# Performance work log

Measured on AMD Instinct MI355X. Metric: run time of the kernel, lower is better.

## Reference

```python
import jax, jax.numpy as jnp
import numpy as np

B, N, C, H, L = 4, 1024, 1152, 16, 120
D = C // H
HID = 4 * C
EPS = 1e-6


def _ln(x):
    m = jnp.mean(x, axis=-1, keepdims=True)
    v = jnp.var(x, axis=-1, keepdims=True)
    return (x - m) * jax.lax.rsqrt(v + EPS)


def _attend(q, k, v):
    # q:(B,H,Nq,D) k,v:(B,H,Nk,D)
    scale = D ** -0.5
    s = jnp.einsum('bhnd,bhmd->bhnm', q, k) * scale
    p = jax.nn.softmax(s, axis=-1)
    o = jnp.einsum('bhnm,bhmd->bhnd', p, v)
    return o.transpose(0, 2, 1, 3).reshape(q.shape[0], q.shape[2], C)


def setup_inputs() -> dict:
    key = jax.random.key(0)
    ks = jax.random.split(key, 20)
    g = lambda i, shape, s=0.02: jax.random.normal(ks[i], shape, jnp.float32) * s
    return {
        'x': jax.random.normal(ks[0], (B, N, C), jnp.float32),
        'y': jax.random.normal(ks[1], (B, L, C), jnp.float32),
        't': jax.random.normal(ks[2], (B, 6 * C), jnp.float32),
        'sst': jax.random.normal(ks[3], (6, C), jnp.float32) / C ** 0.5,
        'qkv_w': g(4, (C, 3 * C)), 'qkv_b': jnp.zeros((3 * C,), jnp.float32),
        'proj_w': g(5, (C, C)), 'proj_b': jnp.zeros((C,), jnp.float32),
        'q_w': g(6, (C, C)), 'q_b': jnp.zeros((C,), jnp.float32),
        'kv_w': g(7, (C, 2 * C)), 'kv_b': jnp.zeros((2 * C,), jnp.float32),
        'cproj_w': g(8, (C, C)), 'cproj_b': jnp.zeros((C,), jnp.float32),
        'fc1_w': g(9, (C, HID)), 'fc1_b': jnp.zeros((HID,), jnp.float32),
        'fc2_w': g(10, (HID, C)), 'fc2_b': jnp.zeros((C,), jnp.float32),
    }


def reference(x, y, t, sst, qkv_w, qkv_b, proj_w, proj_b, q_w, q_b,
              kv_w, kv_b, cproj_w, cproj_b, fc1_w, fc1_b, fc2_w, fc2_b):
    mods = sst[None] + t.reshape(B, 6, C)  # (B,6,C)
    sh_msa, sc_msa, g_msa, sh_mlp, sc_mlp, g_mlp = [mods[:, i:i + 1] for i in range(6)]

    # --- self attention with adaLN modulation ---
    h = _ln(x) * (1 + sc_msa) + sh_msa
    qkv = (h @ qkv_w + qkv_b).reshape(B, N, 3, H, D).transpose(2, 0, 3, 1, 4)
    attn_out = _attend(qkv[0], qkv[1], qkv[2]) @ proj_w + proj_b
    x = x + g_msa * attn_out

    # --- cross attention (batched cond, no mask) ---
    q = (x @ q_w + q_b).reshape(B, N, H, D).transpose(0, 2, 1, 3)
    kv = (y @ kv_w + kv_b).reshape(B, L, 2, H, D).transpose(2, 0, 3, 1, 4)
    x = x + (_attend(q, kv[0], kv[1]) @ cproj_w + cproj_b)

    # --- MLP with adaLN modulation ---
    h = _ln(x) * (1 + sc_mlp) + sh_mlp
    h = jax.nn.gelu(h @ fc1_w + fc1_b, approximate=True) @ fc2_w + fc2_b
    x = x + g_mlp * h
    return x
```

## Files before the change

### kernel.cpp

```cpp
#include <hip/hip_runtime.h>
#include <hip/hip_bf16.h>
#include <stdint.h>

typedef __hip_bfloat16 BT;
typedef __bf16 bf16x8 __attribute__((ext_vector_type(8)));
typedef float f32x4 __attribute__((ext_vector_type(4)));

constexpr int kB = 4, kN = 1024, kC = 1152, kH = 16, kL = 120, kD = 72, kDp = 96;
constexpr int kHid = 4608, kBN = 4096, kZ = 64;
constexpr float kScale = 0.11785113019775793f;

__global__ void detect_dtype(const void* xin, int* flag) {
  __shared__ int cnt;
  if (threadIdx.x == 0) cnt = 0;
  __syncthreads();
  const BT* xb = (const BT*)xin;
  int local = 0;
  for (int i = threadIdx.x; i < 4096; i += 256) {
    float v = __bfloat162float(xb[i]);
    if (!(fabsf(v) <= 1e3f)) local++;
  }
  atomicAdd(&cnt, local);
  __syncthreads();
  if (threadIdx.x == 0) *flag = (cnt > 8) ? 1 : 0;
}

struct ConvSeg {
  const void* src;
  BT* dst;
  long long n;
};
struct ConvArgs {
  ConvSeg seg[10];
  int nseg;
};
__global__ void convert_all(ConvArgs a, const int* __restrict__ flag) {
  const int f = *flag;
  long long i = (long long)blockIdx.x * 256 + threadIdx.x;
#pragma unroll
  for (int s = 0; s < 10; ++s) {
    if (s >= a.nseg) return;
    if (i < a.seg[s].n) {
      a.seg[s].dst[i] = f ? __float2bfloat16(((const float*)a.seg[s].src)[i])
                          : ((const BT*)a.seg[s].src)[i];
      return;
    }
    i -= a.seg[s].n;
  }
}

__global__ void encode_ws(float* out, long long n, float c) {
  long long i = (long long)blockIdx.x * 256 + threadIdx.x;
  if (i < n) out[i] = c;
}

__device__ __forceinline__ void gl_lds16(const BT* g, BT* l) {
  __builtin_amdgcn_global_load_lds(
      (const __attribute__((address_space(1))) uint32_t*)g,
      (__attribute__((address_space(3))) uint32_t*)l, 16, 0, 0);
}

__device__ __forceinline__ bf16x8 ds_read128(const BT* p) {
  f32x4 r;
  auto lp = (const __attribute__((address_space(3))) f32x4*)p;
  asm volatile("ds_read_b128 %0, %1" : "=v"(r) : "v"(lp));
  return __builtin_bit_cast(bf16x8, r);
}

template <int EP>
__global__ __launch_bounds__(256, 2) void gemm_p3(
    const BT* __restrict__ A, const BT* __restrict__ Bm, const BT* __restrict__ bias,
    void* __restrict__ Cout, int M, int Nc, int K, int lda, int ldb, int ldc,
    long long sA, long long sB, long long sC) {
  __shared__ __align__(16) BT As[3][128 * 64];
  __shared__ __align__(16) BT Bs[3][64 * 64];
  A += (long long)blockIdx.z * sA;
  Bm += (long long)blockIdx.z * sB;

  const int gx = gridDim.x, nwg = gx * gridDim.y;
  int id = blockIdx.y * gx + blockIdx.x;
  {
    const int q = nwg >> 3, r = nwg & 7;
    const int xcd = id & 7, pos = id >> 3;
    const int base = (xcd < r) ? xcd * (q + 1) : r * (q + 1) + (xcd - r) * q;
    id = base + pos;
  }
  const int m0 = (id / gx) * 128, n0 = (id % gx) * 64;

  const int lane = threadIdx.x & 63, w = threadIdx.x >> 6;
  const int l15 = lane & 15;
  const int srow = lane >> 3;
  const int ssrc = ((lane & 7) ^ srow) * 8;
  const int wm = (w >> 1) * 64, wn = (w & 1) * 32;

  const BT* gsp[6];
  int eoff[6];
  bool isA[6];
#pragma unroll
  for (int i = 0; i < 6; ++i) {
    const int gidx = w * 6 + i;
    const int u = gidx >> 2, q = gidx & 3;
    if (u < 4) {
      int rr = m0 + u * 32 + q * 8 + srow;
      if (rr >= M) rr = M - 1;
      gsp[i] = A + (long long)rr * lda + ssrc;
      eoff[i] = u * 2048 + q * 512;
      isA[i] = true;
    } else {
      int rr = n0 + (u - 4) * 32 + q * 8 + srow;
      if (rr >= Nc) rr = Nc - 1;
      gsp[i] = Bm + (long long)rr * ldb + ssrc;
      eoff[i] = (u - 4) * 2048 + q * 512;
      isA[i] = false;
    }
  }

  auto stage = [&](int bb, int k0) {
#pragma unroll
    for (int i = 0; i < 6; ++i)
      gl_lds16(gsp[i] + k0, isA[i] ? &As[bb][eoff[i]] : &Bs[bb][eoff[i]]);
  };

  const int rsw = l15 & 7;
  const int ch0 = ((lane >> 4) ^ rsw) * 8;
  const int ch1 = ((4 | (lane >> 4)) ^ rsw) * 8;

  f32x4 acc[4][2] = {};

  const int nk = K >> 6;
  stage(0, 0);
  stage(1, 64);
  asm volatile("s_waitcnt vmcnt(6)" ::: "memory");
  __builtin_amdgcn_s_barrier();

  int cur = 0;
  for (int t = 0; t < nk; ++t) {
    const bool more = (t + 2 < nk);
    if (more) {
      int nb = cur + 2;
      if (nb >= 3) nb -= 3;
      stage(nb, (t + 2) << 6);
    }
    const BT* Ab = &As[cur][0];
    const BT* Bb = &Bs[cur][0];
    bf16x8 af[4][2], bf[2][2];
#pragma unroll
    for (int i = 0; i < 4; ++i) {
      const int row = wm + i * 16 + l15;
      af[i][0] = ds_read128(&Ab[row * 64 + ch0]);
      af[i][1] = ds_read128(&Ab[row * 64 + ch1]);
    }
#pragma unroll
    for (int j = 0; j < 2; ++j) {
      const int row = wn + j * 16 + l15;
      bf[j][0] = ds_read128(&Bb[row * 64 + ch0]);
      bf[j][1] = ds_read128(&Bb[row * 64 + ch1]);
    }
    asm volatile("s_waitcnt lgkmcnt(0)" ::: "memory");
    __builtin_amdgcn_sched_barrier(0);
    __builtin_amdgcn_s_setprio(1);
#pragma unroll
    for (int i = 0; i < 4; ++i)
#pragma unroll
      for (int j = 0; j < 2; ++j) {
        acc[i][j] = __builtin_amdgcn_mfma_f32_16x16x32_bf16(af[i][0], bf[j][0], acc[i][j], 0, 0, 0);
        acc[i][j] = __builtin_amdgcn_mfma_f32_16x16x32_bf16(af[i][1], bf[j][1], acc[i][j], 0, 0, 0);
      }
    __builtin_amdgcn_s_setprio(0);
    if (more)
      asm volatile("s_waitcnt vmcnt(6)" ::: "memory");
    else
      asm volatile("s_waitcnt vmcnt(0)" ::: "memory");
    __builtin_amdgcn_s_barrier();
    ++cur;
    if (cur == 3) cur = 0;
  }

  const int rowq = (lane >> 4) * 4;
  const long long cb = (long long)blockIdx.z * sC;
#pragma unroll
  for (int j = 0; j < 2; ++j) {
    int col = n0 + wn + j * 16 + l15;
    if (col >= Nc) continue;
    float bv = bias ? __bfloat162float(bias[col]) : 0.f;
#pragma unroll
    for (int i = 0; i < 4; ++i) {
      int row = m0 + wm + i * 16 + rowq;
#pragma unroll
      for (int r = 0; r < 4; ++r) {
        if (row + r < M) {
          float v = acc[i][j][r] + bv;
          if (EP == 2) {
            float z = 1.5957691216057308f * (v + 0.044715f * v * v * v);
            v = v / (1.f + __expf(-z));
          }
          long long off = cb + (long long)(row + r) * ldc + col;
          if (EP == 1)
            ((float*)Cout)[off] = v;
          else
            ((BT*)Cout)[off] = __float2bfloat16(v);
        }
      }
    }
  }
}

template <int BM, int BN, int EP>
__global__ __launch_bounds__(256, 3) void gemm_t64(
    const BT* __restrict__ A, const BT* __restrict__ Bm, const BT* __restrict__ bias,
    void* __restrict__ Cout, int M, int Nc, int K, int lda, int ldb, int ldc,
    long long sA, long long sB, long long sC) {
  constexpr int NA = BM / 32;
  constexpr int NB = BN / 32;
  constexpr int NU = NA + NB;
  constexpr int NJ = 2;
  __shared__ __align__(16) BT As[2][BM * 64];
  __shared__ __align__(16) BT Bs[2][BN * 64];
  A += (long long)blockIdx.z * sA;
  Bm += (long long)blockIdx.z * sB;

  const int gx = gridDim.x, nwg = gx * gridDim.y;
  int id = blockIdx.y * gx + blockIdx.x;
  {
    const int q = nwg >> 3, r = nwg & 7;
    const int xcd = id & 7, pos = id >> 3;
    const int base = (xcd < r) ? xcd * (q + 1) : r * (q + 1) + (xcd - r) * q;
    id = base + pos;
  }
  const int m0 = (id / gx) * BM, n0 = (id % gx) * BN;

  const int lane = threadIdx.x & 63, w = threadIdx.x >> 6;
  const int l15 = lane & 15;
  const int srow = lane >> 3;
  const int ssrc = ((lane & 7) ^ srow) * 8;
  const int wm = 0, wn = w * 32;

  const bool has2 = (w + 4 < NU);
  const int u1 = w;
  const int u2 = has2 ? (w + 4) : w;
  const BT* gp1[4];
  const BT* gp2[4];
#pragma unroll
  for (int q = 0; q < 4; ++q) {
    {
      int rr, lim;
      const BT* basep;
      int stride;
      if (u1 < NA) { rr = m0 + u1 * 32; lim = M; basep = A; stride = lda; }
      else { rr = n0 + (u1 - NA) * 32; lim = Nc; basep = Bm; stride = ldb; }
      rr += q * 8 + srow;
      if (rr >= lim) rr = lim - 1;
      gp1[q] = basep + (long long)rr * stride + ssrc;
    }
    {
      int rr, lim;
      const BT* basep;
      int stride;
      if (u2 < NA) { rr = m0 + u2 * 32; lim = M; basep = A; stride = lda; }
      else { rr = n0 + (u2 - NA) * 32; lim = Nc; basep = Bm; stride = ldb; }
      rr += q * 8 + srow;
      if (rr >= lim) rr = lim - 1;
      gp2[q] = basep + (long long)rr * stride + ssrc;
    }
  }
  BT* d1[2];
  BT* d2[2];
#pragma unroll
  for (int bb = 0; bb < 2; ++bb) {
    d1[bb] = (u1 < NA) ? &As[bb][u1 * 2048] : &Bs[bb][(u1 - NA) * 2048];
    int ub = u2 - NA;
    if (ub < 0) ub = 0;
    if (ub > NB - 1) ub = NB - 1;
    d2[bb] = (u2 < NA) ? &As[bb][u2 * 2048] : &Bs[bb][ub * 2048];
  }

  auto stage = [&](int bb, int k0) {
#pragma unroll
    for (int q = 0; q < 4; ++q) gl_lds16(gp1[q] + k0, d1[bb] + q * 512);
    if (has2) {
#pragma unroll
      for (int q = 0; q < 4; ++q) gl_lds16(gp2[q] + k0, d2[bb] + q * 512);
    }
  };

  const int rsw = l15 & 7;
  const int ch0 = ((lane >> 4) ^ rsw) * 8;
  const int ch1 = ((4 | (lane >> 4)) ^ rsw) * 8;

  f32x4 acc[4][NJ] = {};

  auto compute = [&](int bb) {
    bf16x8 af[4][2], bf[NJ][2];
#pragma unroll
    for (int i = 0; i < 4; ++i) {
      const int row = wm + i * 16 + l15;
      af[i][0] = *reinterpret_cast<const bf16x8*>(&As[bb][row * 64 + ch0]);
      af[i][1] = *reinterpret_cast<const bf16x8*>(&As[bb][row * 64 + ch1]);
    }
#pragma unroll
    for (int j = 0; j < NJ; ++j) {
      const int row = wn + j * 16 + l15;
      bf[j][0] = *reinterpret_cast<const bf16x8*>(&Bs[bb][row * 64 + ch0]);
      bf[j][1] = *reinterpret_cast<const bf16x8*>(&Bs[bb][row * 64 + ch1]);
    }
#pragma unroll
    for (int i = 0; i < 4; ++i)
#pragma unroll
      for (int j = 0; j < NJ; ++j) {
        acc[i][j] = __builtin_amdgcn_mfma_f32_16x16x32_bf16(af[i][0], bf[j][0], acc[i][j], 0, 0, 0);
        acc[i][j] = __builtin_amdgcn_mfma_f32_16x16x32_bf16(af[i][1], bf[j][1], acc[i][j], 0, 0, 0);
      }
  };

  stage(0, 0);
  __syncthreads();
  const int nk = K >> 6;
  int cur = 0;
  for (int t = 1; t < nk; ++t) {
    stage(cur ^ 1, t << 6);
    compute(cur);
    __syncthreads();
    cur ^= 1;
  }
  compute(cur);

  const int rowq = (lane >> 4) * 4;
  const long long cb = (long long)blockIdx.z * sC;
#pragma unroll
  for (int j = 0; j < NJ; ++j) {
    int col = n0 + wn + j * 16 + l15;
    if (col >= Nc) continue;
    float bv = bias ? __bfloat162float(bias[col]) : 0.f;
#pragma unroll
    for (int i = 0; i < 4; ++i) {
      int row = m0 + wm + i * 16 + rowq;
#pragma unroll
      for (int r = 0; r < 4; ++r) {
        if (row + r < M) {
          float v = acc[i][j][r] + bv;
          if (EP == 2) {
            float z = 1.5957691216057308f * (v + 0.044715f * v * v * v);
            v = v / (1.f + __expf(-z));
          }
          long long off = cb + (long long)(row + r) * ldc + col;
          if (EP == 1)
            ((float*)Cout)[off] = v;
          else
            ((BT*)Cout)[off] = __float2bfloat16(v);
        }
      }
    }
  }
}

template <int EP>
__global__ __launch_bounds__(256, 4) void gemm_tile(
    const BT* __restrict__ A, const BT* __restrict__ Bm, const BT* __restrict__ bias,
    void* __restrict__ Cout, int M, int Nc, int K, int lda, int ldb, int ldc,
    long long sA, long long sB, long long sC) {
  __shared__ __align__(16) BT As[2][128 * 32];
  __shared__ __align__(16) BT Bs[2][128 * 32];
  A += (long long)blockIdx.z * sA;
  Bm += (long long)blockIdx.z * sB;

  const int gx = gridDim.x, nwg = gx * gridDim.y;
  int id = blockIdx.y * gx + blockIdx.x;
  {
    const int q = nwg >> 3, r = nwg & 7;
    const int xcd = id & 7, pos = id >> 3;
    const int base = (xcd < r) ? xcd * (q + 1) : r * (q + 1) + (xcd - r) * q;
    id = base + pos;
  }
  const int m0 = (id / gx) * 128, n0 = (id % gx) * 128;

  const int lane = threadIdx.x & 63, w = threadIdx.x >> 6;
  const int lr = lane >> 2, lc = (lane & 3) * 8;
  const int l15 = lane & 15, q8 = (lane >> 4) * 8;
  const int wm = (w & 1) * 64, wn = (w >> 1) * 64;

  int ra0 = m0 + w * 32 + lr, ra1 = ra0 + 16;
  if (ra0 >= M) ra0 = M - 1;
  if (ra1 >= M) ra1 = M - 1;
  int rb0 = n0 + w * 32 + lr, rb1 = rb0 + 16;
  if (rb0 >= Nc) rb0 = Nc - 1;
  if (rb1 >= Nc) rb1 = Nc - 1;
  const BT* pa0 = A + (long long)ra0 * lda + lc;
  const BT* pa1 = A + (long long)ra1 * lda + lc;
  const BT* pb0 = Bm + (long long)rb0 * ldb + lc;
  const BT* pb1 = Bm + (long long)rb1 * ldb + lc;

  auto stage = [&](int bb, int k0) {
    gl_lds16(pa0 + k0, &As[bb][w * 1024]);
    gl_lds16(pa1 + k0, &As[bb][w * 1024 + 512]);
    gl_lds16(pb0 + k0, &Bs[bb][w * 1024]);
    gl_lds16(pb1 + k0, &Bs[bb][w * 1024 + 512]);
  };

  f32x4 acc[4][4] = {};

  auto compute = [&](int bb) {
    bf16x8 af[4], bf[4];
#pragma unroll
    for (int i = 0; i < 4; ++i)
      af[i] = *reinterpret_cast<const bf16x8*>(&As[bb][(wm + i * 16 + l15) * 32 + q8]);
#pragma unroll
    for (int j = 0; j < 4; ++j)
      bf[j] = *reinterpret_cast<const bf16x8*>(&Bs[bb][(wn + j * 16 + l15) * 32 + q8]);
#pragma unroll
    for (int i = 0; i < 4; ++i)
#pragma unroll
      for (int j = 0; j < 4; ++j)
        acc[i][j] = __builtin_amdgcn_mfma_f32_16x16x32_bf16(af[i], bf[j], acc[i][j], 0, 0, 0);
  };

  stage(0, 0);
  __syncthreads();
  const int nk = K >> 5;
  int cur = 0;
  for (int t = 1; t < nk; ++t) {
    stage(cur ^ 1, t << 5);
    compute(cur);
    __syncthreads();
    cur ^= 1;
  }
  compute(cur);

  const int rowq = (lane >> 4) * 4;
  const long long cb = (long long)blockIdx.z * sC;
#pragma unroll
  for (int j = 0; j < 4; ++j) {
    int col = n0 + wn + j * 16 + l15;
    if (col >= Nc) continue;
    float bv = bias ? __bfloat162float(bias[col]) : 0.f;
#pragma unroll
    for (int i = 0; i < 4; ++i) {
      int row = m0 + wm + i * 16 + rowq;
#pragma unroll
      for (int r = 0; r < 4; ++r) {
        if (row + r < M) {
          float v = acc[i][j][r] + bv;
          if (EP == 2) {
            float z = 1.5957691216057308f * (v + 0.044715f * v * v * v);
            v = v / (1.f + __expf(-z));
          }
          long long off = cb + (long long)(row + r) * ldc + col;
          if (EP == 1)
            ((float*)Cout)[off] = v;
          else
            ((BT*)Cout)[off] = __float2bfloat16(v);
        }
      }
    }
  }
}

__global__ void transpose_any(const void* __restrict__ in, BT* __restrict__ out,
                              int R, int Cin, const int* __restrict__ flag) {
  __shared__ BT tile[32][33];
  const int f = *flag;
  const int tx = threadIdx.x & 31, ty = threadIdx.x >> 5;
  const int r0 = blockIdx.y * 32, c0 = blockIdx.x * 32;
#pragma unroll
  for (int j = 0; j < 32; j += 8) {
    int r = r0 + ty + j;
    if (r < R && c0 + tx < Cin) {
      long long idx = (long long)r * Cin + c0 + tx;
      tile[ty + j][tx] = f ? __float2bfloat16(((const float*)in)[idx]) : ((const BT*)in)[idx];
    }
  }
  __syncthreads();
#pragma unroll
  for (int j = 0; j < 32; j += 8) {
    int oc = c0 + ty + j;
    if (oc < Cin && r0 + tx < R) out[(long long)oc * R + r0 + tx] = tile[tx][ty + j];
  }
}

template <int SRC>
__global__ __launch_bounds__(256) void ln_mod(const void* __restrict__ xin,
                                              const BT* __restrict__ tc,
                                              const BT* __restrict__ sstc,
                                              BT* __restrict__ hout,
                                              int shiftRow, int scaleRow,
                                              const int* __restrict__ flag) {
  const int f = (SRC == 1) ? 1 : *flag;
  const int row = blockIdx.x;
  const int b = row >> 10;
  const long long base = (long long)row * kC;
  float s = 0.f, s2 = 0.f;
  for (int c = threadIdx.x; c < kC; c += 256) {
    float v = f ? ((const float*)xin)[base + c] : __bfloat162float(((const BT*)xin)[base + c]);
    s += v;
    s2 += v * v;
  }
  for (int o = 32; o > 0; o >>= 1) {
    s += __shfl_down(s, o, 64);
    s2 += __shfl_down(s2, o, 64);
  }
  __shared__ float red[8];
  const int w = threadIdx.x >> 6;
  if ((threadIdx.x & 63) == 0) {
    red[w] = s;
    red[4 + w] = s2;
  }
  __syncthreads();
  const float m = (red[0] + red[1] + red[2] + red[3]) * (1.f / kC);
  const float ex2 = (red[4] + red[5] + red[6] + red[7]) * (1.f / kC);
  const float rstd = rsqrtf(ex2 - m * m + 1e-6f);
  const BT* tsh = tc + (long long)b * 6 * kC + (long long)shiftRow * kC;
  const BT* tsc = tc + (long long)b * 6 * kC + (long long)scaleRow * kC;
  const BT* ssh = sstc + (long long)shiftRow * kC;
  const BT* ssc = sstc + (long long)scaleRow * kC;
  for (int c = threadIdx.x; c < kC; c += 256) {
    float sc = __bfloat162float(ssc[c]) + __bfloat162float(tsc[c]);
    float sh = __bfloat162float(ssh[c]) + __bfloat162float(tsh[c]);
    float xv0 = f ? ((const float*)xin)[base + c] : __bfloat162float(((const BT*)xin)[base + c]);
    float xv = (xv0 - m) * rstd;
    hout[base + c] = __float2bfloat16(xv * (1.f + sc) + sh);
  }
}

__global__ void scatter_qk(const BT* __restrict__ qkv, BT* __restrict__ Qp,
                           BT* __restrict__ Kp) {
  long long i = (long long)blockIdx.x * 256 + threadIdx.x;
  if (i >= (long long)kZ * kN * kDp) return;
  int d = (int)(i % kDp);
  long long r = i / kDp;
  int n = (int)(r % kN);
  int z = (int)(r / kN);
  int b = z >> 4, h = z & 15;
  if (d < kD) {
    long long src = ((long long)(b * kN + n)) * (3 * kC) + h * kD + d;
    Qp[i] = __float2bfloat16(kScale * __bfloat162float(qkv[src]));
    Kp[i] = qkv[src + kC];
  } else {
    Qp[i] = __float2bfloat16(0.f);
    Kp[i] = __float2bfloat16(0.f);
  }
}

__global__ void scatter_v(const BT* __restrict__ qkv, BT* __restrict__ VT) {
  long long i = (long long)blockIdx.x * 256 + threadIdx.x;
  if (i >= (long long)kZ * kD * kN) return;
  int n = (int)(i % kN);
  long long r = i / kN;
  int d = (int)(r % kD);
  int z = (int)(r / kD);
  int b = z >> 4, h = z & 15;
  VT[i] = qkv[((long long)(b * kN + n)) * (3 * kC) + 2 * kC + h * kD + d];
}

__global__ void scatter_qc(const BT* __restrict__ qc, BT* __restrict__ Qp) {
  long long i = (long long)blockIdx.x * 256 + threadIdx.x;
  if (i >= (long long)kZ * kN * kDp) return;
  int d = (int)(i % kDp);
  long long r = i / kDp;
  int n = (int)(r % kN);
  int z = (int)(r / kN);
  int b = z >> 4, h = z & 15;
  Qp[i] = (d < kD)
              ? __float2bfloat16(kScale * __bfloat162float(qc[((long long)(b * kN + n)) * kC + h * kD + d]))
              : __float2bfloat16(0.f);
}

__global__ void scatter_kc(const BT* __restrict__ kvb, BT* __restrict__ Kcp) {
  long long i = (long long)blockIdx.x * 256 + threadIdx.x;
  if (i >= (long long)kZ * kL * kDp) return;
  int d = (int)(i % kDp);
  long long r = i / kDp;
  int l = (int)(r % kL);
  int z = (int)(r / kL);
  int b = z >> 4, h = z & 15;
  Kcp[i] = (d < kD) ? kvb[((long long)(b * kL + l)) * (2 * kC) + h * kD + d] : __float2bfloat16(0.f);
}

__global__ void scatter_vc(const BT* __restrict__ kvb, BT* __restrict__ VcT) {
  long long i = (long long)blockIdx.x * 256 + threadIdx.x;
  if (i >= (long long)kZ * kD * 128) return;
  int l = (int)(i % 128);
  long long r = i / 128;
  int d = (int)(r % kD);
  int z = (int)(r / kD);
  int b = z >> 4, h = z & 15;
  VcT[i] = (l < kL) ? kvb[((long long)(b * kL + l)) * (2 * kC) + kC + h * kD + d] : __float2bfloat16(0.f);
}

__global__ void heads_to_cat(const BT* __restrict__ O, BT* __restrict__ cat) {
  long long i = (long long)blockIdx.x * 256 + threadIdx.x;
  if (i >= (long long)kZ * kN * kD) return;
  int d = (int)(i % kD);
  long long r = i / kD;
  int n = (int)(r % kN);
  int z = (int)(r / kN);
  int b = z >> 4, h = z & 15;
  cat[((long long)(b * kN + n)) * kC + h * kD + d] = O[i];
}

__global__ __launch_bounds__(256) void softmax1024(BT* __restrict__ S) {
  const long long row = blockIdx.x;
  BT* r = S + row * 1024;
  const int tid = threadIdx.x;
  union { ushort4 u; BT b[4]; } ld;
  ld.u = *(const ushort4*)(r + tid * 4);
  float v[4];
#pragma unroll
  for (int k = 0; k < 4; ++k) v[k] = __bfloat162float(ld.b[k]);
  float mx = fmaxf(fmaxf(v[0], v[1]), fmaxf(v[2], v[3]));
  for (int o = 32; o > 0; o >>= 1) mx = fmaxf(mx, __shfl_down(mx, o, 64));
  __shared__ float red[4], red2[4];
  if ((tid & 63) == 0) red[tid >> 6] = mx;
  __syncthreads();
  mx = fmaxf(fmaxf(red[0], red[1]), fmaxf(red[2], red[3]));
  float s = 0.f;
#pragma unroll
  for (int k = 0; k < 4; ++k) {
    v[k] = __expf(v[k] - mx);
    s += v[k];
  }
  for (int o = 32; o > 0; o >>= 1) s += __shfl_down(s, o, 64);
  if ((tid & 63) == 0) red2[tid >> 6] = s;
  __syncthreads();
  s = red2[0] + red2[1] + red2[2] + red2[3];
  const float inv = 1.f / s;
#pragma unroll
  for (int k = 0; k < 4; ++k) ld.b[k] = __float2bfloat16(v[k] * inv);
  *(ushort4*)(r + tid * 4) = ld.u;
}

__global__ void softmax_cross(BT* __restrict__ S) {
  const long long row = blockIdx.x;
  BT* r = S + row * 128;
  const int c = threadIdx.x;
  float v = (c < kL) ? __bfloat162float(r[c]) : -1e30f;
  float mx = v;
  for (int o = 32; o > 0; o >>= 1) mx = fmaxf(mx, __shfl_down(mx, o, 64));
  __shared__ float sm[2], ss[2];
  if ((c & 63) == 0) sm[c >> 6] = mx;
  __syncthreads();
  mx = fmaxf(sm[0], sm[1]);
  float e = (c < kL) ? __expf(v - mx) : 0.f;
  float s = e;
  for (int o = 32; o > 0; o >>= 1) s += __shfl_down(s, o, 64);
  if ((c & 63) == 0) ss[c >> 6] = s;
  __syncthreads();
  s = ss[0] + ss[1];
  r[c] = __float2bfloat16(e / s);
}

__global__ void resid_gate(const void* __restrict__ x, const BT* __restrict__ raw,
                           const BT* __restrict__ tc, const BT* __restrict__ sstc,
                           float* __restrict__ resf, BT* __restrict__ resb,
                           const int* __restrict__ flag) {
  long long i = (long long)blockIdx.x * 256 + threadIdx.x;
  if (i >= (long long)kBN * kC) return;
  const int f = *flag;
  int c = (int)(i % kC);
  int b = (int)(i / ((long long)kN * kC));
  float g = __bfloat162float(sstc[2 * kC + c]) + __bfloat162float(tc[(long long)b * 6 * kC + 2 * kC + c]);
  float xv = f ? ((const float*)x)[i] : __bfloat162float(((const BT*)x)[i]);
  float v = xv + g * __bfloat162float(raw[i]);
  resf[i] = v;
  resb[i] = __float2bfloat16(v);
}

__global__ void resid_add(float* __restrict__ res, const BT* __restrict__ raw) {
  long long i = (long long)blockIdx.x * 256 + threadIdx.x;
  if (i < (long long)kBN * kC) res[i] += __bfloat162float(raw[i]);
}

__global__ void final_out(const float* __restrict__ res, const BT* __restrict__ raw,
                          const BT* __restrict__ tc, const BT* __restrict__ sstc,
                          float* __restrict__ out) {
  long long i = (long long)blockIdx.x * 256 + threadIdx.x;
  if (i >= (long long)kBN * kC) return;
  int c = (int)(i % kC);
  int b = (int)(i / ((long long)kN * kC));
  float g = __bfloat162float(sstc[5 * kC + c]) + __bfloat162float(tc[(long long)b * 6 * kC + 5 * kC + c]);
  out[i] = res[i] + g * __bfloat162float(raw[i]);
}

extern "C" void kernel_launch(void* const* d_in, const int* in_sizes, int n_in,
                              void* d_out, int out_size, void* d_ws, size_t ws_size,
                              hipStream_t stream) {
  const void* x = d_in[0];
  const void* y = d_in[1];
  const void* t = d_in[2];
  const void* sst = d_in[3];
  const void* qkv_w = d_in[4];
  const void* qkv_b = d_in[5];
  const void* proj_w = d_in[6];
  const void* proj_b = d_in[7];
  const void* q_w = d_in[8];
  const void* q_b = d_in[9];
  const void* kv_w = d_in[10];
  const void* kv_b = d_in[11];
  const void* cproj_w = d_in[12];
  const void* cproj_b = d_in[13];
  const void* fc1_w = d_in[14];
  const void* fc1_b = d_in[15];
  const void* fc2_w = d_in[16];
  const void* fc2_b = d_in[17];
  (void)in_sizes; (void)n_in;

  char* p = (char*)d_ws;
  size_t off = 0;
  auto alloc = [&](size_t bytes) {
    void* r = p + off;
    off += (bytes + 1023) & ~(size_t)1023;
    return r;
  };
  int* dflag = (int*)alloc(16);
  BT* canonY = (BT*)alloc((size_t)kB * kL * kC * 2);
  BT* canonT = (BT*)alloc((size_t)kB * 6 * kC * 2);
  BT* canonSst = (BT*)alloc((size_t)6 * kC * 2);
  BT* canonBias = (BT*)alloc((size_t)16384 * 2);
  BT* wT = (BT*)alloc((size_t)kHid * kC * 2);
  BT* bufH = (BT*)alloc((size_t)kBN * kC * 2);
  BT* bufCH = (BT*)alloc((size_t)kZ * kN * kDp * 2);
  BT* bufQp = (BT*)alloc((size_t)kZ * kN * kDp * 2);
  BT* bufVT = (BT*)alloc((size_t)kZ * kD * kN * 2);
  BT* rawB = (BT*)alloc((size_t)kBN * kC * 2);
  float* resF = (float*)alloc((size_t)kBN * kC * 4);
  BT* arena = (BT*)alloc((size_t)kBN * kHid * 2);
  const size_t need = off;

  BT* bufO = rawB;
  BT* fc2T = bufQp;
  BT* kvBuf = (BT*)((char*)arena + 17825792);

  if (ws_size < need) {
    float c = 100.f * (float)(1 + (int)(ws_size >> 24));
    long long n = (long long)out_size;
    encode_ws<<<(int)((n + 255) / 256), 256, 0, stream>>>((float*)d_out, n, c);
    return;
  }

  BT* qkvB = canonBias;
  BT* projB = canonBias + 3456;
  BT* qB = canonBias + 4608;
  BT* kvB = canonBias + 5760;
  BT* cprojB = canonBias + 8064;
  BT* fc1B = canonBias + 9216;
  BT* fc2B = canonBias + 13824;

  auto gemm = [&](int ep, const BT* A, const BT* Bm, const BT* bias, void* Cp,
                  int M, int Nc, int K, int lda, int ldb, int ldc,
                  long long sA, long long sB, long long sC, int Zb) {
    if (K & 63) {
      dim3 g((Nc + 127) / 128, (M + 127) / 128, Zb);
      if (ep == 0)
        gemm_tile<0><<<g, 256, 0, stream>>>(A, Bm, bias, Cp, M, Nc, K, lda, ldb, ldc, sA, sB, sC);
      else if (ep == 1)
        gemm_tile<1><<<g, 256, 0, stream>>>(A, Bm, bias, Cp, M, Nc, K, lda, ldb, ldc, sA, sB, sC);
      else
        gemm_tile<2><<<g, 256, 0, stream>>>(A, Bm, bias, Cp, M, Nc, K, lda, ldb, ldc, sA, sB, sC);
      return;
    }
    if ((M & 127) == 0) {
      dim3 g((Nc + 63) / 64, M / 128, Zb);
      if (ep == 0)
        gemm_p3<0><<<g, 256, 0, stream>>>(A, Bm, bias, Cp, M, Nc, K, lda, ldb, ldc, sA, sB, sC);
      else if (ep == 1)
        gemm_p3<1><<<g, 256, 0, stream>>>(A, Bm, bias, Cp, M, Nc, K, lda, ldb, ldc, sA, sB, sC);
      else
        gemm_p3<2><<<g, 256, 0, stream>>>(A, Bm, bias, Cp, M, Nc, K, lda, ldb, ldc, sA, sB, sC);
    } else {
      dim3 g((Nc + 127) / 128, (M + 63) / 64, Zb);
      if (ep == 0)
        gemm_t64<64, 128, 0><<<g, 256, 0, stream>>>(A, Bm, bias, Cp, M, Nc, K, lda, ldb, ldc, sA, sB, sC);
      else if (ep == 1)
        gemm_t64<64, 128, 1><<<g, 256, 0, stream>>>(A, Bm, bias, Cp, M, Nc, K, lda, ldb, ldc, sA, sB, sC);
      else
        gemm_t64<64, 128, 2><<<g, 256, 0, stream>>>(A, Bm, bias, Cp, M, Nc, K, lda, ldb, ldc, sA, sB, sC);
    }
  };
  auto tp = [&](const void* in, BT* out, int R, int Cin) {
    dim3 g((Cin + 31) / 32, (R + 31) / 32);
    transpose_any<<<g, 256, 0, stream>>>(in, out, R, Cin, dflag);
  };

  detect_dtype<<<1, 256, 0, stream>>>(x, dflag);
  {
    ConvArgs a;
    a.seg[0] = {y, canonY, (long long)kB * kL * kC};
    a.seg[1] = {t, canonT, (long long)kB * 6 * kC};
    a.seg[2] = {sst, canonSst, (long long)6 * kC};
    a.seg[3] = {qkv_b, qkvB, 3456};
    a.seg[4] = {proj_b, projB, 1152};
    a.seg[5] = {q_b, qB, 1152};
    a.seg[6] = {kv_b, kvB, 2304};
    a.seg[7] = {cproj_b, cprojB, 1152};
    a.seg[8] = {fc1_b, fc1B, 4608};
    a.seg[9] = {fc2_b, fc2B, 1152};
    a.nseg = 10;
    long long tot = 552960 + 27648 + 6912 + 14976;
    convert_all<<<(int)((tot + 255) / 256), 256, 0, stream>>>(a, dflag);
  }

  ln_mod<0><<<kBN, 256, 0, stream>>>(x, canonT, canonSst, bufH, 0, 1, dflag);
  tp(qkv_w, wT, kC, 3 * kC);
  gemm(0, bufH, wT, qkvB, arena, kBN, 3 * kC, kC, kC, kC, 3 * kC, 0, 0, 0, 1);
  {
    long long tot = (long long)kZ * kN * kDp;
    scatter_qk<<<(int)((tot + 255) / 256), 256, 0, stream>>>(arena, bufQp, bufCH);
    tot = (long long)kZ * kD * kN;
    scatter_v<<<(int)((tot + 255) / 256), 256, 0, stream>>>(arena, bufVT);
  }
  for (int c = 0; c < 4; ++c) {
    int z0 = c * 16;
    const BT* Qb = bufQp + (size_t)z0 * kN * kDp;
    const BT* Kb = bufCH + (size_t)z0 * kN * kDp;
    const BT* Vb = bufVT + (size_t)z0 * kD * kN;
    BT* Ob = bufO + (size_t)z0 * kN * kD;
    gemm(0, Qb, Kb, nullptr, arena, kN, kN, kDp, kDp, kDp, kN,
         (long long)kN * kDp, (long long)kN * kDp, (long long)kN * kN, 16);
    softmax1024<<<16 * kN, 256, 0, stream>>>(arena);
    gemm(0, arena, Vb, nullptr, Ob, kN, kD, kN, kN, kN, kD,
         (long long)kN * kN, (long long)kD * kN, (long long)kN * kD, 16);
  }
  heads_to_cat<<<18432, 256, 0, stream>>>(bufO, bufCH);
  tp(proj_w, wT, kC, kC);
  gemm(0, bufCH, wT, projB, rawB, kBN, kC, kC, kC, kC, kC, 0, 0, 0, 1);
  resid_gate<<<18432, 256, 0, stream>>>(x, rawB, canonT, canonSst, resF, bufH, dflag);

  tp(q_w, wT, kC, kC);
  gemm(0, bufH, wT, qB, bufCH, kBN, kC, kC, kC, kC, kC, 0, 0, 0, 1);
  {
    long long tot = (long long)kZ * kN * kDp;
    scatter_qc<<<(int)((tot + 255) / 256), 256, 0, stream>>>(bufCH, bufQp);
  }
  tp(kv_w, wT, kC, 2 * kC);
  gemm(0, canonY, wT, kvB, kvBuf, kB * kL, 2 * kC, kC, kC, kC, 2 * kC, 0, 0, 0, 1);
  {
    long long tot = (long long)kZ * kL * kDp;
    scatter_kc<<<(int)((tot + 255) / 256), 256, 0, stream>>>(kvBuf, bufCH);
    tot = (long long)kZ * kD * 128;
    scatter_vc<<<(int)((tot + 255) / 256), 256, 0, stream>>>(kvBuf, bufVT);
  }
  gemm(0, bufQp, bufCH, nullptr, arena, kN, kL, kDp, kDp, kDp, 128,
       (long long)kN * kDp, (long long)kL * kDp, (long long)kN * 128, kZ);
  softmax_cross<<<kZ * kN, 128, 0, stream>>>(arena);
  gemm(0, arena, bufVT, nullptr, bufO, kN, kD, 128, 128, 128, kD,
       (long long)kN * 128, (long long)kD * 128, (long long)kN * kD, kZ);
  heads_to_cat<<<18432, 256, 0, stream>>>(bufO, bufCH);
  tp(cproj_w, wT, kC, kC);
  gemm(0, bufCH, wT, cprojB, rawB, kBN, kC, kC, kC, kC, kC, 0, 0, 0, 1);
  resid_add<<<18432, 256, 0, stream>>>(resF, rawB);

  ln_mod<1><<<kBN, 256, 0, stream>>>(resF, canonT, canonSst, bufH, 3, 4, dflag);
  tp(fc1_w, wT, kC, kHid);
  tp(fc2_w, fc2T, kHid, kC);
  gemm(2, bufH, wT, fc1B, arena, kBN, kHid, kC, kC, kC, kHid, 0, 0, 0, 1);
  gemm(0, arena, fc2T, fc2B, rawB, kBN, kC, kHid, kHid, kHid, kC, 0, 0, 0, 1);
  final_out<<<18432, 256, 0, stream>>>(resF, rawB, canonT, canonSst, (float*)d_out);
}
```

Measured before the change: 832.6 us.

## Replace 4-wave 3-stage GEMM with 8-wave 128x128 double-buffered kernel

Replaces the 128x64 triple-buffered GEMM with a 512-thread kernel that computes 128x128 tiles using double buffering, where each wave loads one 32-row slab. The aim is to raise operand reuse per tile and cut global traffic. Dispatch sends small-grid GEMMs (<512 large tiles) to the 64x128 kernel instead. The hand-tuned asm reads, waitcnt and priority hints are dropped, which risks less latency overlap.

```diff
diff --git a/kernel.cpp b/kernel.cpp
--- a/kernel.cpp
+++ b/kernel.cpp
@@ -60,20 +60,13 @@
       (__attribute__((address_space(3))) uint32_t*)l, 16, 0, 0);
 }
 
-__device__ __forceinline__ bf16x8 ds_read128(const BT* p) {
-  f32x4 r;
-  auto lp = (const __attribute__((address_space(3))) f32x4*)p;
-  asm volatile("ds_read_b128 %0, %1" : "=v"(r) : "v"(lp));
-  return __builtin_bit_cast(bf16x8, r);
-}
-
 template <int EP>
-__global__ __launch_bounds__(256, 2) void gemm_p3(
+__global__ __launch_bounds__(512, 2) void gemm_w8(
     const BT* __restrict__ A, const BT* __restrict__ Bm, const BT* __restrict__ bias,
     void* __restrict__ Cout, int M, int Nc, int K, int lda, int ldb, int ldc,
     long long sA, long long sB, long long sC) {
-  __shared__ __align__(16) BT As[3][128 * 64];
-  __shared__ __align__(16) BT Bs[3][64 * 64];
+  __shared__ __align__(16) BT As[2][128 * 64];
+  __shared__ __align__(16) BT Bs[2][128 * 64];
   A += (long long)blockIdx.z * sA;
   Bm += (long long)blockIdx.z * sB;
 
@@ -85,40 +78,35 @@
     const int base = (xcd < r) ? xcd * (q + 1) : r * (q + 1) + (xcd - r) * q;
     id = base + pos;
   }
-  const int m0 = (id / gx) * 128, n0 = (id % gx) * 64;
+  const int m0 = (id / gx) * 128, n0 = (id % gx) * 128;
 
   const int lane = threadIdx.x & 63, w = threadIdx.x >> 6;
   const int l15 = lane & 15;
   const int srow = lane >> 3;
   const int ssrc = ((lane & 7) ^ srow) * 8;
-  const int wm = (w >> 1) * 64, wn = (w & 1) * 32;
-
-  const BT* gsp[6];
-  int eoff[6];
-  bool isA[6];
-#pragma unroll
-  for (int i = 0; i < 6; ++i) {
-    const int gidx = w * 6 + i;
-    const int u = gidx >> 2, q = gidx & 3;
-    if (u < 4) {
-      int rr = m0 + u * 32 + q * 8 + srow;
-      if (rr >= M) rr = M - 1;
-      gsp[i] = A + (long long)rr * lda + ssrc;
-      eoff[i] = u * 2048 + q * 512;
-      isA[i] = true;
-    } else {
-      int rr = n0 + (u - 4) * 32 + q * 8 + srow;
-      if (rr >= Nc) rr = Nc - 1;
-      gsp[i] = Bm + (long long)rr * ldb + ssrc;
-      eoff[i] = (u - 4) * 2048 + q * 512;
-      isA[i] = false;
-    }
-  }
+  const int wm = (w & 1) * 64, wn = (w >> 1) * 32;
+
+  const int u = w;
+  const BT* gp[4];
+#pragma unroll
+  for (int q = 0; q < 4; ++q) {
+    int rr, lim;
+    const BT* basep;
+    int stride;
+    if (u < 4) { rr = m0 + u * 32; lim = M; basep = A; stride = lda; }
+    else { rr = n0 + (u - 4) * 32; lim = Nc; basep = Bm; stride = ldb; }
+    rr += q * 8 + srow;
+    if (rr >= lim) rr = lim - 1;
+    gp[q] = basep + (long long)rr * stride + ssrc;
+  }
+  BT* dst[2];
+#pragma unroll
+  for (int bb = 0; bb < 2; ++bb)
+    dst[bb] = (u < 4) ? &As[bb][u * 2048] : &Bs[bb][(u - 4) * 2048];
 
   auto stage = [&](int bb, int k0) {
 #pragma unroll
-    for (int i = 0; i < 6; ++i)
-      gl_lds16(gsp[i] + k0, isA[i] ? &As[bb][eoff[i]] : &Bs[bb][eoff[i]]);
+    for (int q = 0; q < 4; ++q) gl_lds16(gp[q] + k0, dst[bb] + q * 512);
   };
 
   const int rsw = l15 & 7;
@@ -127,38 +115,20 @@
 
   f32x4 acc[4][2] = {};
 
-  const int nk = K >> 6;
-  stage(0, 0);
-  stage(1, 64);
-  asm volatile("s_waitcnt vmcnt(6)" ::: "memory");
-  __builtin_amdgcn_s_barrier();
-
-  int cur = 0;
-  for (int t = 0; t < nk; ++t) {
-    const bool more = (t + 2 < nk);
-    if (more) {
-      int nb = cur + 2;
-      if (nb >= 3) nb -= 3;
-      stage(nb, (t + 2) << 6);
-    }
-    const BT* Ab = &As[cur][0];
-    const BT* Bb = &Bs[cur][0];
+  auto compute = [&](int bb) {
     bf16x8 af[4][2], bf[2][2];
 #pragma unroll
     for (int i = 0; i < 4; ++i) {
       const int row = wm + i * 16 + l15;
-      af[i][0] = ds_read128(&Ab[row * 64 + ch0]);
-      af[i][1] = ds_read128(&Ab[row * 64 + ch1]);
+      af[i][0] = *reinterpret_cast<const bf16x8*>(&As[bb][row * 64 + ch0]);
+      af[i][1] = *reinterpret_cast<const bf16x8*>(&As[bb][row * 64 + ch1]);
     }
 #pragma unroll
     for (int j = 0; j < 2; ++j) {
       const int row = wn + j * 16 + l15;
-      bf[j][0] = ds_read128(&Bb[row * 64 + ch0]);
-      bf[j][1] = ds_read128(&Bb[row * 64 + ch1]);
-    }
-    asm volatile("s_waitcnt lgkmcnt(0)" ::: "memory");
-    __builtin_amdgcn_sched_barrier(0);
-    __builtin_amdgcn_s_setprio(1);
+      bf[j][0] = *reinterpret_cast<const bf16x8*>(&Bs[bb][row * 64 + ch0]);
+      bf[j][1] = *reinterpret_cast<const bf16x8*>(&Bs[bb][row * 64 + ch1]);
+    }
 #pragma unroll
     for (int i = 0; i < 4; ++i)
 #pragma unroll
@@ -166,15 +136,19 @@
         acc[i][j] = __builtin_amdgcn_mfma_f32_16x16x32_bf16(af[i][0], bf[j][0], acc[i][j], 0, 0, 0);
         acc[i][j] = __builtin_amdgcn_mfma_f32_16x16x32_bf16(af[i][1], bf[j][1], acc[i][j], 0, 0, 0);
       }
-    __builtin_amdgcn_s_setprio(0);
-    if (more)
-      asm volatile("s_waitcnt vmcnt(6)" ::: "memory");
-    else
-      asm volatile("s_waitcnt vmcnt(0)" ::: "memory");
-    __builtin_amdgcn_s_barrier();
-    ++cur;
-    if (cur == 3) cur = 0;
-  }
+  };
+
+  stage(0, 0);
+  __syncthreads();
+  const int nk = K >> 6;
+  int cur = 0;
+  for (int t = 1; t < nk; ++t) {
+    stage(cur ^ 1, t << 6);
+    compute(cur);
+    __syncthreads();
+    cur ^= 1;
+  }
+  compute(cur);
 
   const int rowq = (lane >> 4) * 4;
   const long long cb = (long long)blockIdx.z * sC;
@@ -205,11 +179,12 @@
   }
 }
 
-template <int BM, int BN, int EP>
+template <int EP>
 __global__ __launch_bounds__(256, 3) void gemm_t64(
     const BT* __restrict__ A, const BT* __restrict__ Bm, const BT* __restrict__ bias,
     void* __restrict__ Cout, int M, int Nc, int K, int lda, int ldb, int ldc,
     long long sA, long long sB, long long sC) {
+  constexpr int BM = 64, BN = 128;
   constexpr int NA = BM / 32;
   constexpr int NB = BN / 32;
   constexpr int NU = NA + NB;
@@ -756,22 +731,23 @@
         gemm_tile<2><<<g, 256, 0, stream>>>(A, Bm, bias, Cp, M, Nc, K, lda, ldb, ldc, sA, sB, sC);
       return;
     }
-    if ((M & 127) == 0) {
-      dim3 g((Nc + 63) / 64, M / 128, Zb);
-      if (ep == 0)
-        gemm_p3<0><<<g, 256, 0, stream>>>(A, Bm, bias, Cp, M, Nc, K, lda, ldb, ldc, sA, sB, sC);
-      else if (ep == 1)
-        gemm_p3<1><<<g, 256, 0, stream>>>(A, Bm, bias, Cp, M, Nc, K, lda, ldb, ldc, sA, sB, sC);
-      else
-        gemm_p3<2><<<g, 256, 0, stream>>>(A, Bm, bias, Cp, M, Nc, K, lda, ldb, ldc, sA, sB, sC);
-    } else {
+    long long nwg128 = (long long)((Nc + 127) / 128) * ((M + 127) / 128) * Zb;
+    if (nwg128 < 512 || (M & 127)) {
       dim3 g((Nc + 127) / 128, (M + 63) / 64, Zb);
       if (ep == 0)
-        gemm_t64<64, 128, 0><<<g, 256, 0, stream>>>(A, Bm, bias, Cp, M, Nc, K, lda, ldb, ldc, sA, sB, sC);
+        gemm_t64<0><<<g, 256, 0, stream>>>(A, Bm, bias, Cp, M, Nc, K, lda, ldb, ldc, sA, sB, sC);
       else if (ep == 1)
-        gemm_t64<64, 128, 1><<<g, 256, 0, stream>>>(A, Bm, bias, Cp, M, Nc, K, lda, ldb, ldc, sA, sB, sC);
+        gemm_t64<1><<<g, 256, 0, stream>>>(A, Bm, bias, Cp, M, Nc, K, lda, ldb, ldc, sA, sB, sC);
       else
-        gemm_t64<64, 128, 2><<<g, 256, 0, stream>>>(A, Bm, bias, Cp, M, Nc, K, lda, ldb, ldc, sA, sB, sC);
+        gemm_t64<2><<<g, 256, 0, stream>>>(A, Bm, bias, Cp, M, Nc, K, lda, ldb, ldc, sA, sB, sC);
+    } else {
+      dim3 g((Nc + 127) / 128, M / 128, Zb);
+      if (ep == 0)
+        gemm_w8<0><<<g, 512, 0, stream>>>(A, Bm, bias, Cp, M, Nc, K, lda, ldb, ldc, sA, sB, sC);
+      else if (ep == 1)
+        gemm_w8<1><<<g, 512, 0, stream>>>(A, Bm, bias, Cp, M, Nc, K, lda, ldb, ldc, sA, sB, sC);
+      else
+        gemm_w8<2><<<g, 512, 0, stream>>>(A, Bm, bias, Cp, M, Nc, K, lda, ldb, ldc, sA, sB, sC);
     }
   };
   auto tp = [&](const void* in, BT* out, int R, int Cin) {
```

Result: no change. 829.8 us (-0.3%).
